# Optimization experiments

Hardware: AMD Instinct MI355X
Metric: run time of the kernel (lower is better)

## Reference

```python
import jax, jax.numpy as jnp
import numpy as np

B, S, HID = 2, 2048, 2048
H, G = 32, 8            # query heads, kv heads
D = HID // H            # head_dim = 64
QPG = H // G            # q heads per kv group = 4


def setup_inputs() -> dict:
    key = jax.random.key(0)
    ks = jax.random.split(key, 5)
    sc = 0.02
    return {
        "x": jax.random.normal(ks[0], (B, S, HID), jnp.float32),
        "Wq": jax.random.normal(ks[1], (HID, HID), jnp.float32) * sc,
        "bq": jnp.zeros((HID,), jnp.float32),
        "Wk": jax.random.normal(ks[2], (HID, G * D), jnp.float32) * sc,
        "bk": jnp.zeros((G * D,), jnp.float32),
        "Wv": jax.random.normal(ks[3], (HID, G * D), jnp.float32) * sc,
        "bv": jnp.zeros((G * D,), jnp.float32),
        "Wo": jax.random.normal(ks[4], (HID, HID), jnp.float32) * sc,
        "bo": jnp.zeros((HID,), jnp.float32),
    }


def reference(x, Wq, bq, Wk, bk, Wv, bv, Wo, bo):
    b, s, _ = x.shape
    # projections (weights stored as [in, out])
    q = (x @ Wq + bq).reshape(b, s, G, QPG, D)      # [b,s,g,p,d]
    k = (x @ Wk + bk).reshape(b, s, G, D)           # [b,s,g,d]
    v = (x @ Wv + bv).reshape(b, s, G, D)
    scale = 1.0 / jnp.sqrt(jnp.asarray(D, x.dtype))
    # grouped attention: repeat_interleave of K/V expressed as shared g axis
    scores = jnp.einsum('bsgpd,btgd->bgpst', q, k) * scale  # [b,g,p,s,t]
    w = jax.nn.softmax(scores, axis=-1)
    o = jnp.einsum('bgpst,btgd->bsgpd', w, v)               # [b,s,g,p,d]
    o = o.reshape(b, s, HID)
    return o @ Wo + bo
```

## Files before the change

kernel.cpp:

```cpp
#include <hip/hip_runtime.h>
#include <hip/hip_bf16.h>


typedef __attribute__((ext_vector_type(8))) short shortx8;
typedef __attribute__((ext_vector_type(4))) float floatx4;

#define SEQ 2048
#define QSC 0.1803368801111204f

#if __has_builtin(__builtin_amdgcn_exp2f)
#define EXP2F(x) __builtin_amdgcn_exp2f(x)
#else
#define EXP2F(x) __expf((x) * 0.6931471805599453f)
#endif

__device__ __forceinline__ unsigned short f2bf(float f) {
  union { float f; unsigned u; } a; a.f = f;
  unsigned u = a.u;
  u += 0x7fffu + ((u >> 16) & 1u);
  return (unsigned short)(u >> 16);
}
__device__ __forceinline__ unsigned pk2f(float lo, float hi) {
  union { float f; unsigned u; } a, b; a.f = lo; b.f = hi;
  return ((a.u + 0x8000u) >> 16) | (((b.u + 0x8000u) >> 16) << 16);
}

__device__ __forceinline__ void gload16(const unsigned short* g, unsigned short* l) {
  __builtin_amdgcn_global_load_lds((const __attribute__((address_space(1))) void*)g,
                                   (__attribute__((address_space(3))) void*)l, 16, 0, 0);
}

__global__ void cast_bf16_kernel(const float* __restrict__ x,
                                 unsigned short* __restrict__ out, int n) {
  int i = (blockIdx.x * blockDim.x + threadIdx.x) * 4;
  if (i < n) {
    float4 v = *(const float4*)(x + i);
    ushort4 o;
    o.x = f2bf(v.x); o.y = f2bf(v.y); o.z = f2bf(v.z); o.w = f2bf(v.w);
    *(ushort4*)(out + i) = o;
  }
}

__global__ void transpose_cast_all(const float* __restrict__ Wq,
                                   const float* __restrict__ Wk,
                                   const float* __restrict__ Wv,
                                   const float* __restrict__ Wo,
                                   unsigned short* __restrict__ WT,
                                   unsigned short* __restrict__ WoT) {
  const int z = blockIdx.z;
  const float* W; unsigned short* D; int N; float sc = 1.f;
  if (z == 0)      { W = Wq; D = WT;                N = 2048; sc = QSC; }
  else if (z == 1) { W = Wk; D = WT + 2048 * 2048;  N = 512; }
  else if (z == 2) { W = Wv; D = WT + 2560 * 2048;  N = 512; }
  else             { W = Wo; D = WoT;               N = 2048; }
  if (blockIdx.x * 32 >= N) return;

  __shared__ float tile[32][33];
  int x = blockIdx.x * 32 + threadIdx.x;
  int y0 = blockIdx.y * 32;
  for (int i = 0; i < 32; i += 8)
    tile[threadIdx.y + i][threadIdx.x] = W[(size_t)(y0 + threadIdx.y + i) * N + x];
  __syncthreads();
  int nx = y0 + threadIdx.x;
  int ny = blockIdx.x * 32 + threadIdx.y;
  for (int i = 0; i < 32; i += 8)
    D[(size_t)(ny + i) * 2048 + nx] = f2bf(tile[threadIdx.x][threadIdx.y + i] * sc);
}

__global__ void concat_bias_kernel(const float* __restrict__ bq,
                                   const float* __restrict__ bk,
                                   const float* __restrict__ bv,
                                   float* __restrict__ out) {
  int i = blockIdx.x * 256 + threadIdx.x;
  if (i < 2048) out[i] = bq[i] * QSC;
  else if (i < 2560) out[i] = bk[i - 2048];
  else if (i < 3072) out[i] = bv[i - 2560];
}

template <int MODE>
__global__ __launch_bounds__(256) void gemm_bt(const unsigned short* __restrict__ A,
                                               const unsigned short* __restrict__ BT,
                                               const float* __restrict__ bias,
                                               void* __restrict__ Cout,
                                               unsigned short* __restrict__ Kbuf,
                                               unsigned short* __restrict__ Vt,
                                               int M, int N, int K) {
  __shared__ __align__(16) unsigned short As[128 * 64];
  __shared__ __align__(16) unsigned short Bs[128 * 64];
  const int m0 = blockIdx.x * 128, n0 = blockIdx.y * 128;
  const int tid = threadIdx.x;
  const int lane = tid & 63, wave = tid >> 6;
  const int l15 = lane & 15, quad = lane >> 4;
  const int wm = (wave & 1) * 64, wn = (wave >> 1) * 64;

  const int r8 = lane >> 3;
  const int clog = (lane & 7) ^ r8;
  const unsigned short* aSrc = A + (size_t)(m0 + wave * 32 + r8) * K + clog * 8;
  const unsigned short* bSrc = BT + (size_t)(n0 + wave * 32 + r8) * K + clog * 8;
  unsigned short* aDst = &As[wave * 2048];
  unsigned short* bDst = &Bs[wave * 2048];

  const int s = l15 & 7;
  int aoff[4], boff[4];
#pragma unroll
  for (int i = 0; i < 4; i++) aoff[i] = (wm + i * 16 + l15) * 64 + (quad ^ s) * 8;
#pragma unroll
  for (int j = 0; j < 4; j++) boff[j] = (wn + j * 16 + l15) * 64 + (quad ^ s) * 8;

  floatx4 acc[4][4];
#pragma unroll
  for (int i = 0; i < 4; i++)
#pragma unroll
    for (int j = 0; j < 4; j++)
#pragma unroll
      for (int r = 0; r < 4; r++) acc[i][j][r] = 0.f;

  for (int k0 = 0; k0 < K; k0 += 64) {
    __syncthreads();
#pragma unroll
    for (int j = 0; j < 4; j++) {
      gload16(aSrc + (size_t)j * 8 * K + k0, aDst + j * 512);
      gload16(bSrc + (size_t)j * 8 * K + k0, bDst + j * 512);
    }
    __syncthreads();
    {
      shortx8 af[4], bf[4];
#pragma unroll
      for (int i = 0; i < 4; i++) af[i] = *(const shortx8*)&As[aoff[i]];
#pragma unroll
      for (int j = 0; j < 4; j++) bf[j] = *(const shortx8*)&Bs[boff[j]];
#pragma unroll
      for (int i = 0; i < 4; i++)
#pragma unroll
        for (int j = 0; j < 4; j++)
          acc[i][j] = __builtin_amdgcn_mfma_f32_16x16x32_bf16(af[i], bf[j], acc[i][j], 0, 0, 0);
#pragma unroll
      for (int i = 0; i < 4; i++) af[i] = *(const shortx8*)&As[aoff[i] ^ 32];
#pragma unroll
      for (int j = 0; j < 4; j++) bf[j] = *(const shortx8*)&Bs[boff[j] ^ 32];
#pragma unroll
      for (int i = 0; i < 4; i++)
#pragma unroll
        for (int j = 0; j < 4; j++)
          acc[i][j] = __builtin_amdgcn_mfma_f32_16x16x32_bf16(af[i], bf[j], acc[i][j], 0, 0, 0);
    }
  }

#pragma unroll
  for (int i = 0; i < 4; i++) {
#pragma unroll
    for (int j = 0; j < 4; j++) {
      int col = n0 + wn + j * 16 + l15;
      float bv = bias[col];
#pragma unroll
      for (int r = 0; r < 4; r++) {
        int row = m0 + wm + i * 16 + quad * 4 + r;
        float v = acc[i][j][r] + bv;
        if (MODE == 0) {
          ((float*)Cout)[(size_t)row * N + col] = v;
        } else {
          if (col < 2048) {
            ((unsigned short*)Cout)[(size_t)row * 2048 + col] = f2bf(v);
          } else if (col < 2560) {
            Kbuf[(size_t)row * 512 + (col - 2048)] = f2bf(v);
          } else {
            int g = (col - 2560) >> 6, d = (col - 2560) & 63;
            int b = row >> 11, sidx = row & 2047;
            Vt[(size_t)(((g << 1) | b) * 64 + d) * 2048 + sidx] = f2bf(v);
          }
        }
      }
    }
  }
}

__global__ __launch_bounds__(256) void attn_kernel(const unsigned short* __restrict__ Qb,
                                                   const unsigned short* __restrict__ Kb,
                                                   const unsigned short* __restrict__ Vt,
                                                   unsigned short* __restrict__ O,
                                                   int h0) {
  const int qt = blockIdx.x, h = h0 + blockIdx.y, b = blockIdx.z;
  const int g = h >> 2;
  const int tid = threadIdx.x;
  const int lane = tid & 63, wave = tid >> 6;
  const int l15 = lane & 15, quad = lane >> 4;

  __shared__ __align__(16) unsigned short Ks[64 * 64];
  __shared__ __align__(16) unsigned short Vs[64 * 64];
  __shared__ __align__(16) unsigned short Ps[4 * 32 * 64];

  const int qrowA = b * SEQ + qt * 128 + wave * 32 + l15;
  const unsigned short* qpA = Qb + (size_t)qrowA * 2048 + h * 64 + quad * 8;
  shortx8 qA0 = *(const shortx8*)qpA;
  shortx8 qA1 = *(const shortx8*)(qpA + 32);
  shortx8 qB0 = *(const shortx8*)(qpA + 16 * 2048);
  shortx8 qB1 = *(const shortx8*)(qpA + 16 * 2048 + 32);

  const int r8 = lane >> 3;
  const int clog = (lane & 7) ^ r8;
  const unsigned short* kSrc = Kb + ((size_t)b * SEQ + wave * 16 + r8) * 512 + g * 64 + clog * 8;
  const unsigned short* vSrc = Vt + ((size_t)(((g << 1) | b) * 64) + wave * 16 + r8) * 2048 + clog * 8;
  unsigned short* kDst = &Ks[wave * 1024];
  unsigned short* vDst = &Vs[wave * 1024];

  const int s = l15 & 7;
  int foff[4];
#pragma unroll
  for (int i = 0; i < 4; i++) foff[i] = (i * 16 + l15) * 64 + (quad ^ s) * 8;

  const int pbaseA = wave * 2048 + l15 * 64;
  const int pbaseB = pbaseA + 16 * 64;
  int pw[4];
#pragma unroll
  for (int i = 0; i < 4; i++) pw[i] = (((i * 2 + (quad >> 1)) ^ s) * 8) + (quad & 1) * 4;
  int pr[2];
#pragma unroll
  for (int ks = 0; ks < 2; ks++) pr[ks] = ((ks * 4 + quad) ^ s) * 8;

  shortx8 ones;
#pragma unroll
  for (int j = 0; j < 8; j++) ones[j] = (short)0x3F80;

  floatx4 oA[4], oB[4], lAacc, lBacc;
#pragma unroll
  for (int nd = 0; nd < 4; nd++)
#pragma unroll
    for (int r = 0; r < 4; r++) { oA[nd][r] = 0.f; oB[nd][r] = 0.f; }
#pragma unroll
  for (int r = 0; r < 4; r++) { lAacc[r] = 0.f; lBacc[r] = 0.f; }

  for (int t0 = 0; t0 < SEQ; t0 += 64) {
    __syncthreads();
    gload16(kSrc + (size_t)t0 * 512, kDst);
    gload16(kSrc + (size_t)(t0 + 8) * 512, kDst + 512);
    gload16(vSrc + t0, vDst);
    gload16(vSrc + (size_t)8 * 2048 + t0, vDst + 512);
    __syncthreads();

    floatx4 sA[4], sB[4];
#pragma unroll
    for (int i = 0; i < 4; i++) {
      shortx8 kf0 = *(const shortx8*)&Ks[foff[i]];
      shortx8 kf1 = *(const shortx8*)&Ks[foff[i] ^ 32];
      floatx4 c = {0.f, 0.f, 0.f, 0.f};
      c = __builtin_amdgcn_mfma_f32_16x16x32_bf16(kf0, qA0, c, 0, 0, 0);
      c = __builtin_amdgcn_mfma_f32_16x16x32_bf16(kf1, qA1, c, 0, 0, 0);
      sA[i] = c;
      floatx4 d = {0.f, 0.f, 0.f, 0.f};
      d = __builtin_amdgcn_mfma_f32_16x16x32_bf16(kf0, qB0, d, 0, 0, 0);
      d = __builtin_amdgcn_mfma_f32_16x16x32_bf16(kf1, qB1, d, 0, 0, 0);
      sB[i] = d;
    }

#pragma unroll
    for (int i = 0; i < 4; i++) {
      float a0 = EXP2F(sA[i][0]), a1 = EXP2F(sA[i][1]);
      float a2 = EXP2F(sA[i][2]), a3 = EXP2F(sA[i][3]);
      uint2 wa; wa.x = pk2f(a0, a1); wa.y = pk2f(a2, a3);
      *(uint2*)&Ps[pbaseA + pw[i]] = wa;
      float b0 = EXP2F(sB[i][0]), b1 = EXP2F(sB[i][1]);
      float b2 = EXP2F(sB[i][2]), b3 = EXP2F(sB[i][3]);
      uint2 wb; wb.x = pk2f(b0, b1); wb.y = pk2f(b2, b3);
      *(uint2*)&Ps[pbaseB + pw[i]] = wb;
    }

#pragma unroll
    for (int ks = 0; ks < 2; ks++) {
      shortx8 pA = *(const shortx8*)&Ps[pbaseA + pr[ks]];
      shortx8 pB = *(const shortx8*)&Ps[pbaseB + pr[ks]];
#pragma unroll
      for (int nd = 0; nd < 4; nd++) {
        shortx8 vf = *(const shortx8*)&Vs[ks ? (foff[nd] ^ 32) : foff[nd]];
        oA[nd] = __builtin_amdgcn_mfma_f32_16x16x32_bf16(vf, pA, oA[nd], 0, 0, 0);
        oB[nd] = __builtin_amdgcn_mfma_f32_16x16x32_bf16(vf, pB, oB[nd], 0, 0, 0);
      }
      lAacc = __builtin_amdgcn_mfma_f32_16x16x32_bf16(ones, pA, lAacc, 0, 0, 0);
      lBacc = __builtin_amdgcn_mfma_f32_16x16x32_bf16(ones, pB, lBacc, 0, 0, 0);
    }
  }

  float iA = 1.f / lAacc[0], iB = 1.f / lBacc[0];
  unsigned short* oPtr = O + (size_t)qrowA * 2048 + h * 64 + quad * 4;
#pragma unroll
  for (int nd = 0; nd < 4; nd++) {
    uint2 w;
    w.x = (unsigned)f2bf(oA[nd][0] * iA) | ((unsigned)f2bf(oA[nd][1] * iA) << 16);
    w.y = (unsigned)f2bf(oA[nd][2] * iA) | ((unsigned)f2bf(oA[nd][3] * iA) << 16);
    *(uint2*)(oPtr + nd * 16) = w;
    uint2 v;
    v.x = (unsigned)f2bf(oB[nd][0] * iB) | ((unsigned)f2bf(oB[nd][1] * iB) << 16);
    v.y = (unsigned)f2bf(oB[nd][2] * iB) | ((unsigned)f2bf(oB[nd][3] * iB) << 16);
    *(uint2*)(oPtr + (size_t)16 * 2048 + nd * 16) = v;
  }
}

extern "C" void kernel_launch(void* const* d_in, const int* in_sizes, int n_in,
                              void* d_out, int out_size, void* d_ws, size_t ws_size,
                              hipStream_t stream) {
  const float* x  = (const float*)d_in[0];
  const float* Wq = (const float*)d_in[1];
  const float* bq = (const float*)d_in[2];
  const float* Wk = (const float*)d_in[3];
  const float* bk = (const float*)d_in[4];
  const float* Wv = (const float*)d_in[5];
  const float* bv = (const float*)d_in[6];
  const float* Wo = (const float*)d_in[7];
  const float* bo = (const float*)d_in[8];
  float* out = (float*)d_out;

  char* ws = (char*)d_ws;
  unsigned short* WTall = (unsigned short*)ws;
  unsigned short* WoT   = (unsigned short*)(ws + 12582912);
  float*          bqkv  = (float*)(ws + 20971520);
  unsigned short* xb    = (unsigned short*)(ws + 20987904);
  unsigned short* Qbuf  = (unsigned short*)(ws + 37765120);
  unsigned short* Kbuf  = (unsigned short*)(ws + 54542336);
  unsigned short* Vt    = (unsigned short*)(ws + 58736640);
  unsigned short* Og    = xb;

  cast_bf16_kernel<<<8192, 256, 0, stream>>>(x, xb, 4096 * 2048);

  transpose_cast_all<<<dim3(64, 64, 4), dim3(32, 8), 0, stream>>>(Wq, Wk, Wv, Wo, WTall, WoT);
  concat_bias_kernel<<<12, 256, 0, stream>>>(bq, bk, bv, bqkv);

  gemm_bt<2><<<dim3(32, 24), 256, 0, stream>>>(xb, WTall, bqkv, Qbuf, Kbuf, Vt, 4096, 3072, 2048);

  attn_kernel<<<dim3(16, 16, 2), 256, 0, stream>>>(Qbuf, Kbuf, Vt, Og, 0);
  attn_kernel<<<dim3(16, 16, 2), 256, 0, stream>>>(Qbuf, Kbuf, Vt, Og, 16);

  gemm_bt<0><<<dim3(32, 16), 256, 0, stream>>>(Og, WoT, bo, out, nullptr, nullptr, 4096, 2048, 2048);
}
```

Baseline: 337.7 us.

## Share K/V tiles across GQA heads in attention and fuse prep kernels

The attention kernel now maps each block to one KV group, with each of its four waves handling one query head and 64 query rows. Every K/V tile loaded into LDS is therefore reused by all four heads of the group instead of being reloaded per head, and the two attention launches become one. The cast, weight transpose and bias concat kernels are merged into a single prep launch to cut launch overhead. In exchange, each wave holds more accumulator registers (16 output fragments) under a launch bound of 2 blocks, and the P buffer in LDS doubles, which may reduce occupancy.

Measured after the change: 322.7 us. 1.05x faster.

```diff
diff --git a/kernel.cpp b/kernel.cpp
--- a/kernel.cpp
+++ b/kernel.cpp
@@ -30,51 +30,55 @@
                                    (__attribute__((address_space(3))) void*)l, 16, 0, 0);
 }
 
-__global__ void cast_bf16_kernel(const float* __restrict__ x,
-                                 unsigned short* __restrict__ out, int n) {
-  int i = (blockIdx.x * blockDim.x + threadIdx.x) * 4;
-  if (i < n) {
-    float4 v = *(const float4*)(x + i);
-    ushort4 o;
-    o.x = f2bf(v.x); o.y = f2bf(v.y); o.z = f2bf(v.z); o.w = f2bf(v.w);
-    *(ushort4*)(out + i) = o;
-  }
-}
-
-__global__ void transpose_cast_all(const float* __restrict__ Wq,
-                                   const float* __restrict__ Wk,
-                                   const float* __restrict__ Wv,
-                                   const float* __restrict__ Wo,
-                                   unsigned short* __restrict__ WT,
-                                   unsigned short* __restrict__ WoT) {
+__global__ void prep_kernel(const float* __restrict__ x,
+                            const float* __restrict__ Wq, const float* __restrict__ Wk,
+                            const float* __restrict__ Wv, const float* __restrict__ Wo,
+                            const float* __restrict__ bq, const float* __restrict__ bk,
+                            const float* __restrict__ bv,
+                            unsigned short* __restrict__ WT,
+                            unsigned short* __restrict__ WoT,
+                            unsigned short* __restrict__ xb,
+                            float* __restrict__ bqkv) {
   const int z = blockIdx.z;
+  if (z == 4) {
+    int fb = blockIdx.y * 64 + blockIdx.x;
+    int tid = threadIdx.y * 32 + threadIdx.x;
+    int i = fb * 2048 + tid * 8;
+    float4 v0 = *(const float4*)(x + i);
+    float4 v1 = *(const float4*)(x + i + 4);
+    ushort4 o0, o1;
+    o0.x = f2bf(v0.x); o0.y = f2bf(v0.y); o0.z = f2bf(v0.z); o0.w = f2bf(v0.w);
+    o1.x = f2bf(v1.x); o1.y = f2bf(v1.y); o1.z = f2bf(v1.z); o1.w = f2bf(v1.w);
+    *(ushort4*)(xb + i) = o0;
+    *(ushort4*)(xb + i + 4) = o1;
+    return;
+  }
+  if (z == 5) {
+    int fb = blockIdx.y * 64 + blockIdx.x;
+    if (fb >= 12) return;
+    int i = fb * 256 + threadIdx.y * 32 + threadIdx.x;
+    if (i < 2048) bqkv[i] = bq[i] * QSC;
+    else if (i < 2560) bqkv[i] = bk[i - 2048];
+    else if (i < 3072) bqkv[i] = bv[i - 2560];
+    return;
+  }
   const float* W; unsigned short* D; int N; float sc = 1.f;
-  if (z == 0)      { W = Wq; D = WT;                N = 2048; sc = QSC; }
-  else if (z == 1) { W = Wk; D = WT + 2048 * 2048;  N = 512; }
-  else if (z == 2) { W = Wv; D = WT + 2560 * 2048;  N = 512; }
-  else             { W = Wo; D = WoT;               N = 2048; }
+  if (z == 0)      { W = Wq; D = WT;               N = 2048; sc = QSC; }
+  else if (z == 1) { W = Wk; D = WT + 2048 * 2048; N = 512; }
+  else if (z == 2) { W = Wv; D = WT + 2560 * 2048; N = 512; }
+  else             { W = Wo; D = WoT;              N = 2048; }
   if (blockIdx.x * 32 >= N) return;
 
   __shared__ float tile[32][33];
-  int x = blockIdx.x * 32 + threadIdx.x;
+  int xx = blockIdx.x * 32 + threadIdx.x;
   int y0 = blockIdx.y * 32;
   for (int i = 0; i < 32; i += 8)
-    tile[threadIdx.y + i][threadIdx.x] = W[(size_t)(y0 + threadIdx.y + i) * N + x];
+    tile[threadIdx.y + i][threadIdx.x] = W[(size_t)(y0 + threadIdx.y + i) * N + xx];
   __syncthreads();
   int nx = y0 + threadIdx.x;
   int ny = blockIdx.x * 32 + threadIdx.y;
   for (int i = 0; i < 32; i += 8)
     D[(size_t)(ny + i) * 2048 + nx] = f2bf(tile[threadIdx.x][threadIdx.y + i] * sc);
-}
-
-__global__ void concat_bias_kernel(const float* __restrict__ bq,
-                                   const float* __restrict__ bk,
-                                   const float* __restrict__ bv,
-                                   float* __restrict__ out) {
-  int i = blockIdx.x * 256 + threadIdx.x;
-  if (i < 2048) out[i] = bq[i] * QSC;
-  else if (i < 2560) out[i] = bk[i - 2048];
-  else if (i < 3072) out[i] = bv[i - 2560];
 }
 
 template <int MODE>
@@ -174,42 +178,43 @@
   }
 }
 
-__global__ __launch_bounds__(256) void attn_kernel(const unsigned short* __restrict__ Qb,
-                                                   const unsigned short* __restrict__ Kb,
-                                                   const unsigned short* __restrict__ Vt,
-                                                   unsigned short* __restrict__ O,
-                                                   int h0) {
-  const int qt = blockIdx.x, h = h0 + blockIdx.y, b = blockIdx.z;
-  const int g = h >> 2;
+__global__ __launch_bounds__(256, 2) void attn_kernel(const unsigned short* __restrict__ Qb,
+                                                      const unsigned short* __restrict__ Kb,
+                                                      const unsigned short* __restrict__ Vt,
+                                                      unsigned short* __restrict__ O) {
+  const int qt = blockIdx.x, g = blockIdx.y, b = blockIdx.z;
   const int tid = threadIdx.x;
   const int lane = tid & 63, wave = tid >> 6;
+  const int h = g * 4 + wave;
   const int l15 = lane & 15, quad = lane >> 4;
 
   __shared__ __align__(16) unsigned short Ks[64 * 64];
   __shared__ __align__(16) unsigned short Vs[64 * 64];
-  __shared__ __align__(16) unsigned short Ps[4 * 32 * 64];
-
-  const int qrowA = b * SEQ + qt * 128 + wave * 32 + l15;
-  const unsigned short* qpA = Qb + (size_t)qrowA * 2048 + h * 64 + quad * 8;
-  shortx8 qA0 = *(const shortx8*)qpA;
-  shortx8 qA1 = *(const shortx8*)(qpA + 32);
-  shortx8 qB0 = *(const shortx8*)(qpA + 16 * 2048);
-  shortx8 qB1 = *(const shortx8*)(qpA + 16 * 2048 + 32);
+  __shared__ __align__(16) unsigned short Ps[4 * 4096];
+
+  shortx8 qf[4][2];
+  {
+    const unsigned short* qp = Qb + (size_t)(b * SEQ + qt * 64 + l15) * 2048 + h * 64 + quad * 8;
+#pragma unroll
+    for (int a = 0; a < 4; a++) {
+      qf[a][0] = *(const shortx8*)(qp + (size_t)a * 16 * 2048);
+      qf[a][1] = *(const shortx8*)(qp + (size_t)a * 16 * 2048 + 32);
+    }
+  }
 
   const int r8 = lane >> 3;
   const int clog = (lane & 7) ^ r8;
   const unsigned short* kSrc = Kb + ((size_t)b * SEQ + wave * 16 + r8) * 512 + g * 64 + clog * 8;
-  const unsigned short* vSrc = Vt + ((size_t)(((g << 1) | b) * 64) + wave * 16 + r8) * 2048 + clog * 8;
+  const unsigned short* vSrc = Vt + ((size_t)((g * 2 + b) * 64 + wave * 16 + r8)) * 2048 + clog * 8;
   unsigned short* kDst = &Ks[wave * 1024];
   unsigned short* vDst = &Vs[wave * 1024];
 
   const int s = l15 & 7;
   int foff[4];
 #pragma unroll
-  for (int i = 0; i < 4; i++) foff[i] = (i * 16 + l15) * 64 + (quad ^ s) * 8;
-
-  const int pbaseA = wave * 2048 + l15 * 64;
-  const int pbaseB = pbaseA + 16 * 64;
+  for (int i = 0; i < 4; i++) foff[i] = (i * 16 + l15) * 64 + ((quad ^ s) * 8);
+
+  const int pbase = wave * 4096 + l15 * 64;
   int pw[4];
 #pragma unroll
   for (int i = 0; i < 4; i++) pw[i] = (((i * 2 + (quad >> 1)) ^ s) * 8) + (quad & 1) * 4;
@@ -221,13 +226,16 @@
 #pragma unroll
   for (int j = 0; j < 8; j++) ones[j] = (short)0x3F80;
 
-  floatx4 oA[4], oB[4], lAacc, lBacc;
-#pragma unroll
-  for (int nd = 0; nd < 4; nd++)
-#pragma unroll
-    for (int r = 0; r < 4; r++) { oA[nd][r] = 0.f; oB[nd][r] = 0.f; }
-#pragma unroll
-  for (int r = 0; r < 4; r++) { lAacc[r] = 0.f; lBacc[r] = 0.f; }
+  floatx4 oacc[4][4], lacc[4];
+#pragma unroll
+  for (int a = 0; a < 4; a++) {
+#pragma unroll
+    for (int r = 0; r < 4; r++) lacc[a][r] = 0.f;
+#pragma unroll
+    for (int nd = 0; nd < 4; nd++)
+#pragma unroll
+      for (int r = 0; r < 4; r++) oacc[a][nd][r] = 0.f;
+  }
 
   for (int t0 = 0; t0 < SEQ; t0 += 64) {
     __syncthreads();
@@ -237,60 +245,61 @@
     gload16(vSrc + (size_t)8 * 2048 + t0, vDst + 512);
     __syncthreads();
 
-    floatx4 sA[4], sB[4];
+    shortx8 kf[4][2];
 #pragma unroll
     for (int i = 0; i < 4; i++) {
-      shortx8 kf0 = *(const shortx8*)&Ks[foff[i]];
-      shortx8 kf1 = *(const shortx8*)&Ks[foff[i] ^ 32];
-      floatx4 c = {0.f, 0.f, 0.f, 0.f};
-      c = __builtin_amdgcn_mfma_f32_16x16x32_bf16(kf0, qA0, c, 0, 0, 0);
-      c = __builtin_amdgcn_mfma_f32_16x16x32_bf16(kf1, qA1, c, 0, 0, 0);
-      sA[i] = c;
-      floatx4 d = {0.f, 0.f, 0.f, 0.f};
-      d = __builtin_amdgcn_mfma_f32_16x16x32_bf16(kf0, qB0, d, 0, 0, 0);
-      d = __builtin_amdgcn_mfma_f32_16x16x32_bf16(kf1, qB1, d, 0, 0, 0);
-      sB[i] = d;
-    }
-
-#pragma unroll
-    for (int i = 0; i < 4; i++) {
-      float a0 = EXP2F(sA[i][0]), a1 = EXP2F(sA[i][1]);
-      float a2 = EXP2F(sA[i][2]), a3 = EXP2F(sA[i][3]);
-      uint2 wa; wa.x = pk2f(a0, a1); wa.y = pk2f(a2, a3);
-      *(uint2*)&Ps[pbaseA + pw[i]] = wa;
-      float b0 = EXP2F(sB[i][0]), b1 = EXP2F(sB[i][1]);
-      float b2 = EXP2F(sB[i][2]), b3 = EXP2F(sB[i][3]);
-      uint2 wb; wb.x = pk2f(b0, b1); wb.y = pk2f(b2, b3);
-      *(uint2*)&Ps[pbaseB + pw[i]] = wb;
-    }
-
-#pragma unroll
-    for (int ks = 0; ks < 2; ks++) {
-      shortx8 pA = *(const shortx8*)&Ps[pbaseA + pr[ks]];
-      shortx8 pB = *(const shortx8*)&Ps[pbaseB + pr[ks]];
-#pragma unroll
-      for (int nd = 0; nd < 4; nd++) {
-        shortx8 vf = *(const shortx8*)&Vs[ks ? (foff[nd] ^ 32) : foff[nd]];
-        oA[nd] = __builtin_amdgcn_mfma_f32_16x16x32_bf16(vf, pA, oA[nd], 0, 0, 0);
-        oB[nd] = __builtin_amdgcn_mfma_f32_16x16x32_bf16(vf, pB, oB[nd], 0, 0, 0);
+      kf[i][0] = *(const shortx8*)&Ks[foff[i]];
+      kf[i][1] = *(const shortx8*)&Ks[foff[i] ^ 32];
+    }
+#pragma unroll
+    for (int a = 0; a < 4; a++) {
+      floatx4 sc[4];
+#pragma unroll
+      for (int i = 0; i < 4; i++) {
+        floatx4 c = {0.f, 0.f, 0.f, 0.f};
+        c = __builtin_amdgcn_mfma_f32_16x16x32_bf16(kf[i][0], qf[a][0], c, 0, 0, 0);
+        c = __builtin_amdgcn_mfma_f32_16x16x32_bf16(kf[i][1], qf[a][1], c, 0, 0, 0);
+        sc[i] = c;
       }
-      lAacc = __builtin_amdgcn_mfma_f32_16x16x32_bf16(ones, pA, lAacc, 0, 0, 0);
-      lBacc = __builtin_amdgcn_mfma_f32_16x16x32_bf16(ones, pB, lBacc, 0, 0, 0);
-    }
-  }
-
-  float iA = 1.f / lAacc[0], iB = 1.f / lBacc[0];
-  unsigned short* oPtr = O + (size_t)qrowA * 2048 + h * 64 + quad * 4;
-#pragma unroll
-  for (int nd = 0; nd < 4; nd++) {
-    uint2 w;
-    w.x = (unsigned)f2bf(oA[nd][0] * iA) | ((unsigned)f2bf(oA[nd][1] * iA) << 16);
-    w.y = (unsigned)f2bf(oA[nd][2] * iA) | ((unsigned)f2bf(oA[nd][3] * iA) << 16);
-    *(uint2*)(oPtr + nd * 16) = w;
-    uint2 v;
-    v.x = (unsigned)f2bf(oB[nd][0] * iB) | ((unsigned)f2bf(oB[nd][1] * iB) << 16);
-    v.y = (unsigned)f2bf(oB[nd][2] * iB) | ((unsigned)f2bf(oB[nd][3] * iB) << 16);
-    *(uint2*)(oPtr + (size_t)16 * 2048 + nd * 16) = v;
+#pragma unroll
+      for (int i = 0; i < 4; i++) {
+        float p0 = EXP2F(sc[i][0]), p1 = EXP2F(sc[i][1]);
+        float p2 = EXP2F(sc[i][2]), p3 = EXP2F(sc[i][3]);
+        uint2 w; w.x = pk2f(p0, p1); w.y = pk2f(p2, p3);
+        *(uint2*)&Ps[pbase + a * 1024 + pw[i]] = w;
+      }
+    }
+
+    shortx8 vf[4][2];
+#pragma unroll
+    for (int nd = 0; nd < 4; nd++) {
+      vf[nd][0] = *(const shortx8*)&Vs[foff[nd]];
+      vf[nd][1] = *(const shortx8*)&Vs[foff[nd] ^ 32];
+    }
+#pragma unroll
+    for (int a = 0; a < 4; a++) {
+#pragma unroll
+      for (int ks = 0; ks < 2; ks++) {
+        shortx8 pf = *(const shortx8*)&Ps[pbase + a * 1024 + pr[ks]];
+#pragma unroll
+        for (int nd = 0; nd < 4; nd++)
+          oacc[a][nd] = __builtin_amdgcn_mfma_f32_16x16x32_bf16(vf[nd][ks], pf, oacc[a][nd], 0, 0, 0);
+        lacc[a] = __builtin_amdgcn_mfma_f32_16x16x32_bf16(ones, pf, lacc[a], 0, 0, 0);
+      }
+    }
+  }
+
+#pragma unroll
+  for (int a = 0; a < 4; a++) {
+    float inv = 1.f / lacc[a][0];
+    unsigned short* oPtr = O + (size_t)(b * SEQ + qt * 64 + a * 16 + l15) * 2048 + h * 64 + quad * 4;
+#pragma unroll
+    for (int nd = 0; nd < 4; nd++) {
+      uint2 w;
+      w.x = (unsigned)f2bf(oacc[a][nd][0] * inv) | ((unsigned)f2bf(oacc[a][nd][1] * inv) << 16);
+      w.y = (unsigned)f2bf(oacc[a][nd][2] * inv) | ((unsigned)f2bf(oacc[a][nd][3] * inv) << 16);
+      *(uint2*)(oPtr + nd * 16) = w;
+    }
   }
 }
 
@@ -318,15 +327,12 @@
   unsigned short* Vt    = (unsigned short*)(ws + 58736640);
   unsigned short* Og    = xb;
 
-  cast_bf16_kernel<<<8192, 256, 0, stream>>>(x, xb, 4096 * 2048);
-
-  transpose_cast_all<<<dim3(64, 64, 4), dim3(32, 8), 0, stream>>>(Wq, Wk, Wv, Wo, WTall, WoT);
-  concat_bias_kernel<<<12, 256, 0, stream>>>(bq, bk, bv, bqkv);
+  prep_kernel<<<dim3(64, 64, 6), dim3(32, 8), 0, stream>>>(
+      x, Wq, Wk, Wv, Wo, bq, bk, bv, WTall, WoT, xb, bqkv);
 
   gemm_bt<2><<<dim3(32, 24), 256, 0, stream>>>(xb, WTall, bqkv, Qbuf, Kbuf, Vt, 4096, 3072, 2048);
 
-  attn_kernel<<<dim3(16, 16, 2), 256, 0, stream>>>(Qbuf, Kbuf, Vt, Og, 0);
-  attn_kernel<<<dim3(16, 16, 2), 256, 0, stream>>>(Qbuf, Kbuf, Vt, Og, 16);
+  attn_kernel<<<dim3(32, 8, 2), 256, 0, stream>>>(Qbuf, Kbuf, Vt, Og);
 
   gemm_bt<0><<<dim3(32, 16), 256, 0, stream>>>(Og, WoT, bo, out, nullptr, nullptr, 4096, 2048, 2048);
 }
```
